# Kernel tuning notes

Measured on AMD Instinct MI355X. Metric: run time of the kernel, lower is better.

## Reference

```python
import jax, jax.numpy as jnp
import numpy as np

DIM = 128; HEADS = 8; WS = 8; SHIFT = 4; B = 8; H = 256; W = 256; T = 1


def _rel_index(ws):
    # faithful port of create_relative_position_index
    coords = np.arange(ws)
    yy, xx = np.meshgrid(coords, coords, indexing='ij')
    cf = np.stack([yy.reshape(-1), xx.reshape(-1)])          # (2, ws*ws)
    rel = cf[:, :, None] - cf[:, None, :]                     # (2, N, N)
    rel[0] += ws - 1
    rel[1] += ws - 1
    return rel[0] * (2 * ws - 1) + rel[1]                     # (N, N) int


def _row_mask(ws, shift):
    jj, ii = np.meshgrid(np.arange(ws), np.arange(ws), indexing='ij')
    return ((jj >= ws - shift) | (ii >= ws - shift)).reshape(-1)  # (N,) bool


def layernorm(x, g, b, eps=1e-5):
    mu = x.mean(-1, keepdims=True)
    var = ((x - mu) ** 2).mean(-1, keepdims=True)
    return (x - mu) * jax.lax.rsqrt(var + eps) * g + b


def setup_inputs() -> dict:
    key = jax.random.key(0)
    ks = jax.random.split(key, 16)
    s = 0.02
    d = DIM
    inp = {
        'x': jax.random.normal(ks[0], (B, T, H, W, d), jnp.float32),
        'wq': jax.random.normal(ks[1], (d, d), jnp.float32) * s,
        'bq': jnp.zeros((d,), jnp.float32),
        'wk': jax.random.normal(ks[2], (d, d), jnp.float32) * s,
        'bk': jnp.zeros((d,), jnp.float32),
        'wv': jax.random.normal(ks[3], (d, d), jnp.float32) * s,
        'bv': jnp.zeros((d,), jnp.float32),
        'wp': jax.random.normal(ks[4], (d, d), jnp.float32) * s,
        'bp': jnp.zeros((d,), jnp.float32),
        'rpb': jax.random.normal(ks[5], (2 * WS - 1, 2 * WS - 1, HEADS), jnp.float32) * s,
        'ln1_g': jnp.ones((d,), jnp.float32),
        'ln1_b': jnp.zeros((d,), jnp.float32),
        'ln2_g': jnp.ones((d,), jnp.float32),
        'ln2_b': jnp.zeros((d,), jnp.float32),
        'w1': jax.random.normal(ks[6], (d, 4 * d), jnp.float32) * s,
        'b1': jnp.zeros((4 * d,), jnp.float32),
        'w2': jax.random.normal(ks[7], (4 * d, d), jnp.float32) * s,
        'b2': jnp.zeros((d,), jnp.float32),
        'gate': jax.random.normal(ks[8], (1, H, W, 1), jnp.float32) * s,
    }
    return inp


def reference(x, wq, bq, wk, bk, wv, bv, wp, bp, rpb, ln1_g, ln1_b, ln2_g, ln2_b, w1, b1, w2, b2, gate):
    Bx, Tx, Hx, Wx, C = x.shape
    skip = x[:, 0]                                             # (B,H,W,C)
    xn = layernorm(x, ln1_g, ln1_b)[:, 0]                      # (B,H,W,C)
    xs = jnp.roll(xn, (-SHIFT, -SHIFT), axis=(1, 2))
    nh, nw, N = Hx // WS, Wx // WS, WS * WS
    # window partition -> (B*nh*nw, N, C)
    xw = xs.reshape(Bx, nh, WS, nw, WS, C).transpose(0, 1, 3, 2, 4, 5).reshape(-1, N, C)
    hd = C // HEADS
    scale = hd ** -0.5
    q = (xw @ wq + bq).reshape(-1, N, HEADS, hd)
    k = (xw @ wk + bk).reshape(-1, N, HEADS, hd)
    v = (xw @ wv + bv).reshape(-1, N, HEADS, hd)
    attn = jnp.einsum('bnhc,bmhc->bnhm', q, k) * scale         # (Bw,N,H,N)
    # relative position bias gather; .view(B,N,heads,N) over (N*N,heads) flat layout
    idx = jnp.asarray(_rel_index(WS).reshape(-1))
    bias = rpb.reshape(-1, HEADS)[idx].reshape(N, HEADS, N)
    attn = attn + bias[None]
    # shift mask: full query rows set to -1e9 (per original patch_mask)
    rmask = jnp.asarray(_row_mask(WS, SHIFT))
    attn = jnp.where(rmask[None, :, None, None], jnp.float32(-1e9), attn)
    attn = jax.nn.softmax(attn, axis=-1)
    out = jnp.einsum('bnhm,bmhc->bnhc', attn, v).reshape(-1, N, C) @ wp + bp
    # window reverse
    xr = out.reshape(Bx, nh, nw, WS, WS, C).transpose(0, 1, 3, 2, 4, 5).reshape(Bx, Hx, Wx, C)
    xa = xs + xr
    xa = jnp.roll(xa, (SHIFT, SHIFT), axis=(1, 2))
    # gated skip
    x2 = xa + jax.nn.sigmoid(gate) * skip
    # MLP (dropout = identity in eval)
    h = jax.nn.gelu(layernorm(x2, ln2_g, ln2_b) @ w1 + b1, approximate=False)
    y = x2 + (h @ w2 + b2)
    return y.reshape(Bx, Tx, Hx, Wx, C)
```

## Files before the change

kernel.cpp:

```cpp
#include <hip/hip_runtime.h>
#include <hip/hip_bf16.h>
#include <math.h>

#define TPB 256

typedef __attribute__((ext_vector_type(8))) __bf16 bf16x8;
typedef __attribute__((ext_vector_type(4))) __bf16 bf16x4;
typedef __attribute__((ext_vector_type(4))) float f32x4;

static __device__ __forceinline__ bf16x8 lds_frag(const char* base, int row, int byteOff, int rowBytes) {
    return *reinterpret_cast<const bf16x8*>(base + row * rowBytes + (byteOff ^ ((row & 7) << 4)));
}
static __device__ __forceinline__ void lds_wr4(char* base, int row, int col0, int rowBytes, f32x4 v) {
    bf16x4 p;
    p[0] = (__bf16)v[0]; p[1] = (__bf16)v[1]; p[2] = (__bf16)v[2]; p[3] = (__bf16)v[3];
    *reinterpret_cast<bf16x4*>(base + row * rowBytes + ((col0 << 1) ^ ((row & 7) << 4))) = p;
}

__global__ void convert_w(const float* __restrict__ wq, const float* __restrict__ wk,
                          const float* __restrict__ wv, const float* __restrict__ wp,
                          const float* __restrict__ w1, const float* __restrict__ w2,
                          const float* __restrict__ rpb, const float* __restrict__ bq,
                          __bf16* __restrict__ ws)
{
    int g = blockIdx.x * 256 + threadIdx.x;
    if (g < 65536) {
        int which = g >> 14, idx = g & 16383, n = idx >> 7, k = idx & 127;
        const float* W = (which == 0) ? wq : (which == 1) ? wk : (which == 2) ? wv : wp;
        float v = W[k * 128 + n];
        if (which == 0) v *= 0.25f;
        ws[g] = (__bf16)v;
    } else if (g < 131072) {
        int idx = g - 65536, n = idx >> 7, k = idx & 127;
        ws[g] = (__bf16)w1[k * 512 + n];
    } else if (g < 196608) {
        int idx = g - 131072, n = idx >> 9, k = idx & 511;
        ws[g] = (__bf16)w2[k * 128 + n];
    } else if (g < 204800) {
        float* wsf = (float*)(ws + 196608);
        int g2 = g - 196608;
        int hc = g2 >> 8, h = hc >> 2, ct = hc & 3;
        int lane = (g2 >> 2) & 63, kg = lane >> 4, ar = lane & 15, r = g2 & 3;
        int dy = (ar >> 2) - h + 7;
        int dx = (ar & 3) - (ct * 2 + (kg >> 1)) + 7;
        int hsrc = ((kg & 1) << 2) | r;
        wsf[g2] = rpb[(dy * 15 + dx) * 8 + hsrc];
    } else if (g < 204928) {
        float* wsf = (float*)(ws + 196608);
        wsf[8192 + (g - 204800)] = bq[g - 204800] * 0.25f;
    }
}

#define O_P     4096
#define O_ATTN  12288
#define O_MU    49152
#define O_RS    49408
#define O_GATE  49664
#define O_BASE  49920
#define O_VMEAN 50176
#define SMEM_SZ 50688

__global__ __launch_bounds__(TPB, 3) void swin_fused_kernel(
    const float* __restrict__ x,
    const __bf16* __restrict__ wqT,
    const __bf16* __restrict__ wkT, const float* __restrict__ bk,
    const __bf16* __restrict__ wvT, const float* __restrict__ bv,
    const __bf16* __restrict__ wpT, const float* __restrict__ bp,
    const float* __restrict__ bias_pre, const float* __restrict__ bqs,
    const float* __restrict__ ln1g, const float* __restrict__ ln1b,
    const float* __restrict__ ln2g, const float* __restrict__ ln2b,
    const __bf16* __restrict__ w1T, const float* __restrict__ b1,
    const __bf16* __restrict__ w2T, const float* __restrict__ b2,
    const float* __restrict__ gate,
    float* __restrict__ out)
{
    __shared__ __align__(16) char smem[SMEM_SZ];
    char* s_xn   = smem;
    char* s_q    = smem;
    char* s_k    = smem + 16384;
    char* s_vT   = smem + 32768;
    char* s_xn2  = smem + 32768;
    char* s_attn = smem + O_ATTN;
    char* s_h    = smem;
    float* s_proj = (float*)(smem);
    float* s_out  = (float*)(smem);
    float* s_mu   = (float*)(smem + O_MU);
    float* s_rs   = (float*)(smem + O_RS);
    float* s_gate = (float*)(smem + O_GATE);
    int*   s_base = (int*)(smem + O_BASE);
    float* s_vmean = (float*)(smem + O_VMEAN);

    const int tid = threadIdx.x;
    const int blk = blockIdx.x;
    const int b  = blk >> 10;
    const int wh = (blk >> 5) & 31;
    const int ww = blk & 31;

    const int row = tid >> 2;
    const int l4  = tid & 3;
    float vals[32];

    {
        const int si = wh * 8 + (row >> 3), sj = ww * 8 + (row & 7);
        const int oi = (si + 4) & 255, oj = (sj + 4) & 255;
        const int base = ((b * 256 + oi) * 256 + oj) * 128;
        if (l4 == 0) { s_base[row] = base; s_gate[row] = gate[oi * 256 + oj]; }
        const float* xp = x + base + l4 * 32;
        float sum = 0.f, sq = 0.f;
#pragma unroll
        for (int i = 0; i < 8; ++i) {
            const float4 v4 = reinterpret_cast<const float4*>(xp)[i];
            vals[4*i+0] = v4.x; vals[4*i+1] = v4.y; vals[4*i+2] = v4.z; vals[4*i+3] = v4.w;
            sum += v4.x + v4.y + v4.z + v4.w;
            sq  += v4.x*v4.x + v4.y*v4.y + v4.z*v4.z + v4.w*v4.w;
        }
        sum += __shfl_xor(sum, 1); sum += __shfl_xor(sum, 2);
        sq  += __shfl_xor(sq , 1); sq  += __shfl_xor(sq , 2);
        const float mu  = sum * (1.f / 128.f);
        const float var = sq * (1.f / 128.f) - mu * mu;
        const float rs  = rsqrtf(var + 1e-5f);
        if (l4 == 0) { s_mu[row] = mu; s_rs[row] = rs; }
#pragma unroll
        for (int j = 0; j < 4; ++j) {
            bf16x8 pk;
#pragma unroll
            for (int e = 0; e < 8; ++e) {
                const int d = l4 * 32 + j * 8 + e;
                pk[e] = (__bf16)((vals[j*8+e] - mu) * rs * ln1g[d] + ln1b[d]);
            }
            const int byteOff = (l4 * 64 + j * 16) ^ ((row & 7) << 4);
            *reinterpret_cast<bf16x8*>(s_xn + row * 256 + byteOff) = pk;
        }
    }
    __syncthreads();

    const int lane = tid & 63, w = tid >> 6;
    const int ar = lane & 15, kg = lane >> 4;

    bf16x8 a[4][4];
    bf16x8 aq[4];
    {
#pragma unroll
        for (int nt = 0; nt < 4; ++nt)
#pragma unroll
            for (int kc = 0; kc < 4; ++kc)
                a[nt][kc] = lds_frag(s_xn, nt * 16 + ar, kc * 64 + (kg << 4), 256);
        const int nrow = ((ar >> 2) << 3) + (ar & 3);
#pragma unroll
        for (int kc = 0; kc < 4; ++kc)
            aq[kc] = lds_frag(s_xn, nrow, kc * 64 + (kg << 4), 256);

#pragma unroll
        for (int ct2 = 0; ct2 < 2; ++ct2) {
            const int m0t = (w + ct2 * 4) * 16;
            bf16x8 af[4];
#pragma unroll
            for (int kc = 0; kc < 4; ++kc)
                af[kc] = *reinterpret_cast<const bf16x8*>(wkT + (m0t + ar) * 128 + kc * 32 + (kg << 3));
            const float4 bb4 = *reinterpret_cast<const float4*>(bk + m0t + kg * 4);
#pragma unroll
            for (int nt = 0; nt < 4; ++nt) {
                f32x4 c = {bb4.x, bb4.y, bb4.z, bb4.w};
#pragma unroll
                for (int kc = 0; kc < 4; ++kc)
                    c = __builtin_amdgcn_mfma_f32_16x16x32_bf16(af[kc], a[nt][kc], c, 0, 0, 0);
                lds_wr4(s_k, nt * 16 + ar, m0t + kg * 4, 256, c);
            }
        }
#pragma unroll
        for (int ct2 = 0; ct2 < 2; ++ct2) {
            const int brow = (w + ct2 * 4) * 16 + ar;
            bf16x8 bf[4];
#pragma unroll
            for (int kc = 0; kc < 4; ++kc)
                bf[kc] = *reinterpret_cast<const bf16x8*>(wvT + brow * 128 + kc * 32 + (kg << 3));
            const float bb = bv[brow];
            float vs = 0.f;
#pragma unroll
            for (int rt = 0; rt < 4; ++rt) {
                f32x4 c = {bb, bb, bb, bb};
#pragma unroll
                for (int kc = 0; kc < 4; ++kc)
                    c = __builtin_amdgcn_mfma_f32_16x16x32_bf16(a[rt][kc], bf[kc], c, 0, 0, 0);
                lds_wr4(s_vT, brow, rt * 16 + kg * 4, 128, c);
                vs += c[0] + c[1] + c[2] + c[3];
            }
            vs += __shfl_xor(vs, 16); vs += __shfl_xor(vs, 32);
            if (kg == 0) s_vmean[brow] = vs * (1.f / 64.f);
        }
    }
    __syncthreads();

    {
#pragma unroll
        for (int ct2 = 0; ct2 < 2; ++ct2) {
            const int m0t = (w + ct2 * 4) * 16;
            bf16x8 af[4];
#pragma unroll
            for (int kc = 0; kc < 4; ++kc)
                af[kc] = *reinterpret_cast<const bf16x8*>(wqT + (m0t + ar) * 128 + kc * 32 + (kg << 3));
            const float4 bb4 = *reinterpret_cast<const float4*>(bqs + m0t + kg * 4);
            f32x4 c = {bb4.x, bb4.y, bb4.z, bb4.w};
#pragma unroll
            for (int kc = 0; kc < 4; ++kc)
                c = __builtin_amdgcn_mfma_f32_16x16x32_bf16(af[kc], aq[kc], c, 0, 0, 0);
            lds_wr4(s_q, ar, m0t + kg * 4, 256, c);
        }
    }
    __syncthreads();

    char* s_p = smem + O_P + (w << 11);
#pragma unroll
    for (int hi = 0; hi < 2; ++hi) {
        const int h = w + hi * 4;
        bf16x8 aQ = {};
        if (lane < 32) aQ = lds_frag(s_q, ar, h * 32 + (kg << 4), 256);
        f32x4 sc[4];
#pragma unroll
        for (int ct = 0; ct < 4; ++ct) {
            bf16x8 bK = {};
            if (lane < 32) bK = lds_frag(s_k, ct * 16 + ar, h * 32 + (kg << 4), 256);
            const f32x4 cin = *reinterpret_cast<const f32x4*>(bias_pre + ((h * 4 + ct) << 8) + (lane << 2));
            sc[ct] = __builtin_amdgcn_mfma_f32_16x16x32_bf16(bK, aQ, cin, 0, 0, 0);
        }
        float sm = 0.f;
#pragma unroll
        for (int ct = 0; ct < 4; ++ct)
#pragma unroll
            for (int r = 0; r < 4; ++r) {
                sc[ct][r] = __expf(sc[ct][r]);
                sm += sc[ct][r];
            }
        sm += __shfl_xor(sm, 16); sm += __shfl_xor(sm, 32);
        const float inv = 1.f / sm;
#pragma unroll
        for (int ct = 0; ct < 4; ++ct) {
            f32x4 p4 = {sc[ct][0] * inv, sc[ct][1] * inv, sc[ct][2] * inv, sc[ct][3] * inv};
            lds_wr4(s_p, ar, ct * 16 + kg * 4, 128, p4);
        }
        f32x4 o = {0.f, 0.f, 0.f, 0.f};
#pragma unroll
        for (int kc = 0; kc < 2; ++kc) {
            bf16x8 ap = lds_frag(s_p,  ar, kc * 64 + (kg << 4), 128);
            bf16x8 bV = lds_frag(s_vT, h * 16 + ar, kc * 64 + (kg << 4), 128);
            o = __builtin_amdgcn_mfma_f32_16x16x32_bf16(bV, ap, o, 0, 0, 0);
        }
        lds_wr4(s_attn, ar, h * 16 + kg * 4, 256, o);
    }
    __syncthreads();

    {
        bf16x8 a2[4];
#pragma unroll
        for (int kc = 0; kc < 4; ++kc)
            a2[kc] = lds_frag(s_attn, ar, kc * 64 + (kg << 4), 256);
#pragma unroll
        for (int ct2 = 0; ct2 < 2; ++ct2) {
            const int brow = (w + ct2 * 4) * 16 + ar;
            bf16x8 bf[4];
#pragma unroll
            for (int kc = 0; kc < 4; ++kc)
                bf[kc] = *reinterpret_cast<const bf16x8*>(wpT + brow * 128 + kc * 32 + (kg << 3));
            const float bb = bp[brow];
            f32x4 c = {bb, bb, bb, bb};
#pragma unroll
            for (int kc = 0; kc < 4; ++kc)
                c = __builtin_amdgcn_mfma_f32_16x16x32_bf16(a2[kc], bf[kc], c, 0, 0, 0);
#pragma unroll
            for (int r = 0; r < 4; ++r)
                s_proj[(kg * 4 + r) * 132 + brow] = c[r];
        }
        if (tid < 128) {
            const int col = tid;
            float acc = bp[col];
#pragma unroll
            for (int j = 0; j < 16; ++j) {
                const bf16x8 w8 = *reinterpret_cast<const bf16x8*>(wpT + col * 128 + j * 8);
#pragma unroll
                for (int e = 0; e < 8; ++e)
                    acc += s_vmean[j * 8 + e] * (float)w8[e];
            }
            s_proj[16 * 132 + col] = acc;
        }
    }
    __syncthreads();

    {
        const float sg = 1.f / (1.f + __expf(-s_gate[row]));
        const float mu1 = s_mu[row], rs1 = s_rs[row];
        const bool masked = ((row >> 3) >= 4) || ((row & 7) >= 4);
        const int prow = masked ? 16 : ((row >> 3) * 4 + (row & 7));
        const float* pr = s_proj + prow * 132 + l4 * 32;
        const float* g1  = ln1g + l4 * 32;
        const float* b1v = ln1b + l4 * 32;
        float sum = 0.f, sq = 0.f;
#pragma unroll
        for (int i = 0; i < 8; ++i) {
            const float4 gg = reinterpret_cast<const float4*>(g1)[i];
            const float4 bb = reinterpret_cast<const float4*>(b1v)[i];
            const float g4[4] = {gg.x, gg.y, gg.z, gg.w};
            const float b4[4] = {bb.x, bb.y, bb.z, bb.w};
#pragma unroll
            for (int c = 0; c < 4; ++c) {
                const int idx = 4*i + c;
                const float xv = vals[idx];
                const float xnv = (xv - mu1) * rs1 * g4[c] + b4[c];
                const float x2 = xnv + pr[idx] + sg * xv;
                vals[idx] = x2;
                sum += x2; sq += x2 * x2;
            }
        }
        sum += __shfl_xor(sum, 1); sum += __shfl_xor(sum, 2);
        sq  += __shfl_xor(sq , 1); sq  += __shfl_xor(sq , 2);
        const float mu  = sum * (1.f / 128.f);
        const float var = sq * (1.f / 128.f) - mu * mu;
        const float rs  = rsqrtf(var + 1e-5f);
        __syncthreads();
#pragma unroll
        for (int j = 0; j < 4; ++j) {
            bf16x8 pk;
#pragma unroll
            for (int e = 0; e < 8; ++e) {
                const int d = l4 * 32 + j * 8 + e;
                pk[e] = (__bf16)((vals[j*8+e] - mu) * rs * ln2g[d] + ln2b[d]);
            }
            const int byteOff = (l4 * 64 + j * 16) ^ ((row & 7) << 4);
            *reinterpret_cast<bf16x8*>(s_xn2 + row * 256 + byteOff) = pk;
        }
    }
    __syncthreads();

    bf16x8 bx[4][4];
#pragma unroll
    for (int nt = 0; nt < 4; ++nt)
#pragma unroll
        for (int kc = 0; kc < 4; ++kc)
            bx[nt][kc] = lds_frag(s_xn2, nt * 16 + ar, kc * 64 + (kg << 4), 256);

    f32x4 acc2[2][4];
#pragma unroll
    for (int ct2 = 0; ct2 < 2; ++ct2) {
        const float bb = b2[(w + ct2 * 4) * 16 + ar];
#pragma unroll
        for (int rt = 0; rt < 4; ++rt) acc2[ct2][rt] = {bb, bb, bb, bb};
    }

#pragma unroll
    for (int hh = 0; hh < 2; ++hh) {
#pragma unroll
        for (int i = 0; i < 4; ++i) {
            const int hcol0 = (w + 4 * i) * 16;
            const int m0g = hh * 256 + hcol0;
            bf16x8 af[4];
#pragma unroll
            for (int kc = 0; kc < 4; ++kc)
                af[kc] = *reinterpret_cast<const bf16x8*>(w1T + (m0g + ar) * 128 + kc * 32 + (kg << 3));
            const float4 bb4 = *reinterpret_cast<const float4*>(b1 + m0g + kg * 4);
#pragma unroll
            for (int nt = 0; nt < 4; ++nt) {
                f32x4 c = {bb4.x, bb4.y, bb4.z, bb4.w};
#pragma unroll
                for (int kc = 0; kc < 4; ++kc)
                    c = __builtin_amdgcn_mfma_f32_16x16x32_bf16(af[kc], bx[nt][kc], c, 0, 0, 0);
                f32x4 g4;
#pragma unroll
                for (int r = 0; r < 4; ++r) {
                    const float v = c[r];
                    const float t = 0.7978845608028654f * (v + 0.044715f * v * v * v);
                    const float th = 1.f - 2.f / (__expf(2.f * t) + 1.f);
                    g4[r] = 0.5f * v * (1.f + th);
                }
                lds_wr4(s_h, nt * 16 + ar, hcol0 + kg * 4, 512, g4);
            }
        }
        __syncthreads();
#pragma unroll
        for (int kc = 0; kc < 8; ++kc) {
            bf16x8 ah[4];
#pragma unroll
            for (int rt = 0; rt < 4; ++rt)
                ah[rt] = lds_frag(s_h, rt * 16 + ar, kc * 64 + (kg << 4), 512);
#pragma unroll
            for (int ct2 = 0; ct2 < 2; ++ct2) {
                const int brow = (w + ct2 * 4) * 16 + ar;
                const bf16x8 bw = *reinterpret_cast<const bf16x8*>(w2T + brow * 512 + hh * 256 + kc * 32 + (kg << 3));
#pragma unroll
                for (int rt = 0; rt < 4; ++rt)
                    acc2[ct2][rt] = __builtin_amdgcn_mfma_f32_16x16x32_bf16(ah[rt], bw, acc2[ct2][rt], 0, 0, 0);
            }
        }
        __syncthreads();
    }

#pragma unroll
    for (int ct2 = 0; ct2 < 2; ++ct2)
#pragma unroll
        for (int rt = 0; rt < 4; ++rt)
#pragma unroll
            for (int r = 0; r < 4; ++r)
                s_out[(rt * 16 + kg * 4 + r) * 132 + (w + ct2 * 4) * 16 + ar] = acc2[ct2][rt][r];
    __syncthreads();
    {
        const int base = s_base[row];
        float* op = out + base + l4 * 32;
        const float* po = s_out + row * 132 + l4 * 32;
#pragma unroll
        for (int i = 0; i < 8; ++i) {
            float4 o;
            o.x = vals[4*i+0] + po[4*i+0];
            o.y = vals[4*i+1] + po[4*i+1];
            o.z = vals[4*i+2] + po[4*i+2];
            o.w = vals[4*i+3] + po[4*i+3];
            reinterpret_cast<float4*>(op)[i] = o;
        }
    }
}

extern "C" void kernel_launch(void* const* d_in, const int* in_sizes, int n_in,
                              void* d_out, int out_size, void* d_ws, size_t ws_size,
                              hipStream_t stream) {
    (void)in_sizes; (void)n_in; (void)ws_size; (void)out_size;
    const float* x    = (const float*)d_in[0];
    const float* wq   = (const float*)d_in[1];
    const float* bq   = (const float*)d_in[2];
    const float* wk   = (const float*)d_in[3];
    const float* bk   = (const float*)d_in[4];
    const float* wv   = (const float*)d_in[5];
    const float* bv   = (const float*)d_in[6];
    const float* wp   = (const float*)d_in[7];
    const float* bp   = (const float*)d_in[8];
    const float* rpb  = (const float*)d_in[9];
    const float* ln1g = (const float*)d_in[10];
    const float* ln1b = (const float*)d_in[11];
    const float* ln2g = (const float*)d_in[12];
    const float* ln2b = (const float*)d_in[13];
    const float* w1   = (const float*)d_in[14];
    const float* b1   = (const float*)d_in[15];
    const float* w2   = (const float*)d_in[16];
    const float* b2   = (const float*)d_in[17];
    const float* gate = (const float*)d_in[18];
    float* out = (float*)d_out;

    __bf16* ws = (__bf16*)d_ws;
    const __bf16* wqT = ws;
    const __bf16* wkT = ws + 16384;
    const __bf16* wvT = ws + 32768;
    const __bf16* wpT = ws + 49152;
    const __bf16* w1T = ws + 65536;
    const __bf16* w2T = ws + 131072;
    const float* wsf  = (const float*)(ws + 196608);
    const float* bias_pre = wsf;
    const float* bqs      = wsf + 8192;

    convert_w<<<801, 256, 0, stream>>>(wq, wk, wv, wp, w1, w2, rpb, bq, ws);
    swin_fused_kernel<<<8192, TPB, 0, stream>>>(x, wqT, wkT, bk, wvT, bv, wpT, bp,
                                                bias_pre, bqs, ln1g, ln1b, ln2g, ln2b,
                                                w1T, b1, w2T, b2, gate, out);
}
```

Before: 745.8 us.

## Double block size to 512 threads, one head per wave, simplified GELU

Doubles the threads per block from 256 to 512 so each of the 8 waves owns one head and one 16-column tile in the QKV, projection and MLP GEMMs. Each thread now handles 16 channels instead of 32. The K and V projections are fused into one loop that reloads activation fragments from LDS per tile instead of keeping a 4x4 fragment array in registers. The smem layout is enlarged so the P buffers no longer alias, and one barrier is removed from the LN2 phase. GELU uses a sigmoid form with a fast reciprocal, and the softmax uses rcp. This is meant to cut register pressure and raise parallelism per window, at the cost of larger LDS use, a lower occupancy bound of 2, and more LDS fragment reads.

Result: slower. 776.7 us (+4.1%).

```diff
diff --git a/kernel.cpp b/kernel.cpp
--- a/kernel.cpp
+++ b/kernel.cpp
@@ -2,7 +2,7 @@
 #include <hip/hip_bf16.h>
 #include <math.h>
 
-#define TPB 256
+#define TPB 512
 
 typedef __attribute__((ext_vector_type(8))) __bf16 bf16x8;
 typedef __attribute__((ext_vector_type(4))) __bf16 bf16x4;
@@ -51,16 +51,18 @@
     }
 }
 
-#define O_P     4096
 #define O_ATTN  12288
-#define O_MU    49152
-#define O_RS    49408
-#define O_GATE  49664
-#define O_BASE  49920
-#define O_VMEAN 50176
-#define SMEM_SZ 50688
-
-__global__ __launch_bounds__(TPB, 3) void swin_fused_kernel(
+#define O_K     16384
+#define O_VT    32768
+#define O_P     49152
+#define O_MU    65536
+#define O_RS    65792
+#define O_GATE  66048
+#define O_BASE  66304
+#define O_VMEAN 66560
+#define SMEM_SZ 67072
+
+__global__ __launch_bounds__(TPB, 2) void swin_fused_kernel(
     const float* __restrict__ x,
     const __bf16* __restrict__ wqT,
     const __bf16* __restrict__ wkT, const float* __restrict__ bk,
@@ -77,10 +79,10 @@
     __shared__ __align__(16) char smem[SMEM_SZ];
     char* s_xn   = smem;
     char* s_q    = smem;
-    char* s_k    = smem + 16384;
-    char* s_vT   = smem + 32768;
-    char* s_xn2  = smem + 32768;
     char* s_attn = smem + O_ATTN;
+    char* s_k    = smem + O_K;
+    char* s_vT   = smem + O_VT;
+    char* s_xn2  = smem + O_VT;
     char* s_h    = smem;
     float* s_proj = (float*)(smem);
     float* s_out  = (float*)(smem);
@@ -96,39 +98,39 @@
     const int wh = (blk >> 5) & 31;
     const int ww = blk & 31;
 
-    const int row = tid >> 2;
-    const int l4  = tid & 3;
-    float vals[32];
+    const int row = tid >> 3;
+    const int l8  = tid & 7;
+    float vals[16];
 
     {
         const int si = wh * 8 + (row >> 3), sj = ww * 8 + (row & 7);
         const int oi = (si + 4) & 255, oj = (sj + 4) & 255;
         const int base = ((b * 256 + oi) * 256 + oj) * 128;
-        if (l4 == 0) { s_base[row] = base; s_gate[row] = gate[oi * 256 + oj]; }
-        const float* xp = x + base + l4 * 32;
+        if (l8 == 0) { s_base[row] = base; s_gate[row] = gate[oi * 256 + oj]; }
+        const float* xp = x + base + l8 * 16;
         float sum = 0.f, sq = 0.f;
 #pragma unroll
-        for (int i = 0; i < 8; ++i) {
+        for (int i = 0; i < 4; ++i) {
             const float4 v4 = reinterpret_cast<const float4*>(xp)[i];
             vals[4*i+0] = v4.x; vals[4*i+1] = v4.y; vals[4*i+2] = v4.z; vals[4*i+3] = v4.w;
             sum += v4.x + v4.y + v4.z + v4.w;
             sq  += v4.x*v4.x + v4.y*v4.y + v4.z*v4.z + v4.w*v4.w;
         }
-        sum += __shfl_xor(sum, 1); sum += __shfl_xor(sum, 2);
-        sq  += __shfl_xor(sq , 1); sq  += __shfl_xor(sq , 2);
+        sum += __shfl_xor(sum, 1); sum += __shfl_xor(sum, 2); sum += __shfl_xor(sum, 4);
+        sq  += __shfl_xor(sq , 1); sq  += __shfl_xor(sq , 2); sq  += __shfl_xor(sq , 4);
         const float mu  = sum * (1.f / 128.f);
         const float var = sq * (1.f / 128.f) - mu * mu;
         const float rs  = rsqrtf(var + 1e-5f);
-        if (l4 == 0) { s_mu[row] = mu; s_rs[row] = rs; }
-#pragma unroll
-        for (int j = 0; j < 4; ++j) {
+        if (l8 == 0) { s_mu[row] = mu; s_rs[row] = rs; }
+#pragma unroll
+        for (int j = 0; j < 2; ++j) {
             bf16x8 pk;
 #pragma unroll
             for (int e = 0; e < 8; ++e) {
-                const int d = l4 * 32 + j * 8 + e;
+                const int d = l8 * 16 + j * 8 + e;
                 pk[e] = (__bf16)((vals[j*8+e] - mu) * rs * ln1g[d] + ln1b[d]);
             }
-            const int byteOff = (l4 * 64 + j * 16) ^ ((row & 7) << 4);
+            const int byteOff = (l8 * 32 + j * 16) ^ ((row & 7) << 4);
             *reinterpret_cast<bf16x8*>(s_xn + row * 256 + byteOff) = pk;
         }
     }
@@ -137,82 +139,66 @@
     const int lane = tid & 63, w = tid >> 6;
     const int ar = lane & 15, kg = lane >> 4;
 
-    bf16x8 a[4][4];
     bf16x8 aq[4];
-    {
-#pragma unroll
-        for (int nt = 0; nt < 4; ++nt)
+
+    {
+        const int nrow = ((ar >> 2) << 3) + (ar & 3);
+#pragma unroll
+        for (int kc = 0; kc < 4; ++kc)
+            aq[kc] = lds_frag(s_xn, nrow, kc * 64 + (kg << 4), 256);
+
+        const int m0t = w * 16;
+        const int brow = w * 16 + ar;
+        bf16x8 afk[4], bfv[4];
+#pragma unroll
+        for (int kc = 0; kc < 4; ++kc) {
+            afk[kc] = *reinterpret_cast<const bf16x8*>(wkT + (m0t + ar) * 128 + kc * 32 + (kg << 3));
+            bfv[kc] = *reinterpret_cast<const bf16x8*>(wvT + brow * 128 + kc * 32 + (kg << 3));
+        }
+        const float4 bbk = *reinterpret_cast<const float4*>(bk + m0t + kg * 4);
+        const float bbv = bv[brow];
+        float vs = 0.f;
+#pragma unroll
+        for (int nt = 0; nt < 4; ++nt) {
+            bf16x8 bx[4];
 #pragma unroll
             for (int kc = 0; kc < 4; ++kc)
-                a[nt][kc] = lds_frag(s_xn, nt * 16 + ar, kc * 64 + (kg << 4), 256);
-        const int nrow = ((ar >> 2) << 3) + (ar & 3);
-#pragma unroll
-        for (int kc = 0; kc < 4; ++kc)
-            aq[kc] = lds_frag(s_xn, nrow, kc * 64 + (kg << 4), 256);
-
-#pragma unroll
-        for (int ct2 = 0; ct2 < 2; ++ct2) {
-            const int m0t = (w + ct2 * 4) * 16;
-            bf16x8 af[4];
+                bx[kc] = lds_frag(s_xn, nt * 16 + ar, kc * 64 + (kg << 4), 256);
+            f32x4 ck = {bbk.x, bbk.y, bbk.z, bbk.w};
 #pragma unroll
             for (int kc = 0; kc < 4; ++kc)
-                af[kc] = *reinterpret_cast<const bf16x8*>(wkT + (m0t + ar) * 128 + kc * 32 + (kg << 3));
-            const float4 bb4 = *reinterpret_cast<const float4*>(bk + m0t + kg * 4);
-#pragma unroll
-            for (int nt = 0; nt < 4; ++nt) {
-                f32x4 c = {bb4.x, bb4.y, bb4.z, bb4.w};
-#pragma unroll
-                for (int kc = 0; kc < 4; ++kc)
-                    c = __builtin_amdgcn_mfma_f32_16x16x32_bf16(af[kc], a[nt][kc], c, 0, 0, 0);
-                lds_wr4(s_k, nt * 16 + ar, m0t + kg * 4, 256, c);
-            }
-        }
-#pragma unroll
-        for (int ct2 = 0; ct2 < 2; ++ct2) {
-            const int brow = (w + ct2 * 4) * 16 + ar;
-            bf16x8 bf[4];
+                ck = __builtin_amdgcn_mfma_f32_16x16x32_bf16(afk[kc], bx[kc], ck, 0, 0, 0);
+            lds_wr4(s_k, nt * 16 + ar, m0t + kg * 4, 256, ck);
+            f32x4 cv = {bbv, bbv, bbv, bbv};
 #pragma unroll
             for (int kc = 0; kc < 4; ++kc)
-                bf[kc] = *reinterpret_cast<const bf16x8*>(wvT + brow * 128 + kc * 32 + (kg << 3));
-            const float bb = bv[brow];
-            float vs = 0.f;
-#pragma unroll
-            for (int rt = 0; rt < 4; ++rt) {
-                f32x4 c = {bb, bb, bb, bb};
-#pragma unroll
-                for (int kc = 0; kc < 4; ++kc)
-                    c = __builtin_amdgcn_mfma_f32_16x16x32_bf16(a[rt][kc], bf[kc], c, 0, 0, 0);
-                lds_wr4(s_vT, brow, rt * 16 + kg * 4, 128, c);
-                vs += c[0] + c[1] + c[2] + c[3];
-            }
-            vs += __shfl_xor(vs, 16); vs += __shfl_xor(vs, 32);
-            if (kg == 0) s_vmean[brow] = vs * (1.f / 64.f);
-        }
-    }
-    __syncthreads();
-
-    {
-#pragma unroll
-        for (int ct2 = 0; ct2 < 2; ++ct2) {
-            const int m0t = (w + ct2 * 4) * 16;
-            bf16x8 af[4];
-#pragma unroll
-            for (int kc = 0; kc < 4; ++kc)
-                af[kc] = *reinterpret_cast<const bf16x8*>(wqT + (m0t + ar) * 128 + kc * 32 + (kg << 3));
-            const float4 bb4 = *reinterpret_cast<const float4*>(bqs + m0t + kg * 4);
-            f32x4 c = {bb4.x, bb4.y, bb4.z, bb4.w};
-#pragma unroll
-            for (int kc = 0; kc < 4; ++kc)
-                c = __builtin_amdgcn_mfma_f32_16x16x32_bf16(af[kc], aq[kc], c, 0, 0, 0);
-            lds_wr4(s_q, ar, m0t + kg * 4, 256, c);
-        }
-    }
-    __syncthreads();
-
-    char* s_p = smem + O_P + (w << 11);
-#pragma unroll
-    for (int hi = 0; hi < 2; ++hi) {
-        const int h = w + hi * 4;
+                cv = __builtin_amdgcn_mfma_f32_16x16x32_bf16(bx[kc], bfv[kc], cv, 0, 0, 0);
+            lds_wr4(s_vT, brow, nt * 16 + kg * 4, 128, cv);
+            vs += cv[0] + cv[1] + cv[2] + cv[3];
+        }
+        vs += __shfl_xor(vs, 16); vs += __shfl_xor(vs, 32);
+        if (kg == 0) s_vmean[brow] = vs * (1.f / 64.f);
+    }
+    __syncthreads();
+
+    {
+        const int m0t = w * 16;
+        bf16x8 af[4];
+#pragma unroll
+        for (int kc = 0; kc < 4; ++kc)
+            af[kc] = *reinterpret_cast<const bf16x8*>(wqT + (m0t + ar) * 128 + kc * 32 + (kg << 3));
+        const float4 bb4 = *reinterpret_cast<const float4*>(bqs + m0t + kg * 4);
+        f32x4 c = {bb4.x, bb4.y, bb4.z, bb4.w};
+#pragma unroll
+        for (int kc = 0; kc < 4; ++kc)
+            c = __builtin_amdgcn_mfma_f32_16x16x32_bf16(af[kc], aq[kc], c, 0, 0, 0);
+        lds_wr4(s_q, ar, m0t + kg * 4, 256, c);
+    }
+    __syncthreads();
+
+    {
+        const int h = w;
+        char* s_p = smem + O_P + (w << 11);
         bf16x8 aQ = {};
         if (lane < 32) aQ = lds_frag(s_q, ar, h * 32 + (kg << 4), 256);
         f32x4 sc[4];
@@ -232,7 +218,7 @@
                 sm += sc[ct][r];
             }
         sm += __shfl_xor(sm, 16); sm += __shfl_xor(sm, 32);
-        const float inv = 1.f / sm;
+        const float inv = __builtin_amdgcn_rcpf(sm);
 #pragma unroll
         for (int ct = 0; ct < 4; ++ct) {
             f32x4 p4 = {sc[ct][0] * inv, sc[ct][1] * inv, sc[ct][2] * inv, sc[ct][3] * inv};
@@ -254,22 +240,19 @@
 #pragma unroll
         for (int kc = 0; kc < 4; ++kc)
             a2[kc] = lds_frag(s_attn, ar, kc * 64 + (kg << 4), 256);
-#pragma unroll
-        for (int ct2 = 0; ct2 < 2; ++ct2) {
-            const int brow = (w + ct2 * 4) * 16 + ar;
-            bf16x8 bf[4];
-#pragma unroll
-            for (int kc = 0; kc < 4; ++kc)
-                bf[kc] = *reinterpret_cast<const bf16x8*>(wpT + brow * 128 + kc * 32 + (kg << 3));
-            const float bb = bp[brow];
-            f32x4 c = {bb, bb, bb, bb};
-#pragma unroll
-            for (int kc = 0; kc < 4; ++kc)
-                c = __builtin_amdgcn_mfma_f32_16x16x32_bf16(a2[kc], bf[kc], c, 0, 0, 0);
-#pragma unroll
-            for (int r = 0; r < 4; ++r)
-                s_proj[(kg * 4 + r) * 132 + brow] = c[r];
-        }
+        const int brow = w * 16 + ar;
+        bf16x8 bf[4];
+#pragma unroll
+        for (int kc = 0; kc < 4; ++kc)
+            bf[kc] = *reinterpret_cast<const bf16x8*>(wpT + brow * 128 + kc * 32 + (kg << 3));
+        const float bb = bp[brow];
+        f32x4 c = {bb, bb, bb, bb};
+#pragma unroll
+        for (int kc = 0; kc < 4; ++kc)
+            c = __builtin_amdgcn_mfma_f32_16x16x32_bf16(a2[kc], bf[kc], c, 0, 0, 0);
+#pragma unroll
+        for (int r = 0; r < 4; ++r)
+            s_proj[(kg * 4 + r) * 132 + brow] = c[r];
         if (tid < 128) {
             const int col = tid;
             float acc = bp[col];
@@ -290,12 +273,12 @@
         const float mu1 = s_mu[row], rs1 = s_rs[row];
         const bool masked = ((row >> 3) >= 4) || ((row & 7) >= 4);
         const int prow = masked ? 16 : ((row >> 3) * 4 + (row & 7));
-        const float* pr = s_proj + prow * 132 + l4 * 32;
-        const float* g1  = ln1g + l4 * 32;
-        const float* b1v = ln1b + l4 * 32;
+        const float* pr = s_proj + prow * 132 + l8 * 16;
+        const float* g1  = ln1g + l8 * 16;
+        const float* b1v = ln1b + l8 * 16;
         float sum = 0.f, sq = 0.f;
 #pragma unroll
-        for (int i = 0; i < 8; ++i) {
+        for (int i = 0; i < 4; ++i) {
             const float4 gg = reinterpret_cast<const float4*>(g1)[i];
             const float4 bb = reinterpret_cast<const float4*>(b1v)[i];
             const float g4[4] = {gg.x, gg.y, gg.z, gg.w};
@@ -310,67 +293,70 @@
                 sum += x2; sq += x2 * x2;
             }
         }
-        sum += __shfl_xor(sum, 1); sum += __shfl_xor(sum, 2);
-        sq  += __shfl_xor(sq , 1); sq  += __shfl_xor(sq , 2);
+        sum += __shfl_xor(sum, 1); sum += __shfl_xor(sum, 2); sum += __shfl_xor(sum, 4);
+        sq  += __shfl_xor(sq , 1); sq  += __shfl_xor(sq , 2); sq  += __shfl_xor(sq , 4);
         const float mu  = sum * (1.f / 128.f);
         const float var = sq * (1.f / 128.f) - mu * mu;
         const float rs  = rsqrtf(var + 1e-5f);
-        __syncthreads();
-#pragma unroll
-        for (int j = 0; j < 4; ++j) {
+#pragma unroll
+        for (int j = 0; j < 2; ++j) {
             bf16x8 pk;
 #pragma unroll
             for (int e = 0; e < 8; ++e) {
-                const int d = l4 * 32 + j * 8 + e;
+                const int d = l8 * 16 + j * 8 + e;
                 pk[e] = (__bf16)((vals[j*8+e] - mu) * rs * ln2g[d] + ln2b[d]);
             }
-            const int byteOff = (l4 * 64 + j * 16) ^ ((row & 7) << 4);
+            const int byteOff = (l8 * 32 + j * 16) ^ ((row & 7) << 4);
             *reinterpret_cast<bf16x8*>(s_xn2 + row * 256 + byteOff) = pk;
         }
     }
     __syncthreads();
 
-    bf16x8 bx[4][4];
-#pragma unroll
-    for (int nt = 0; nt < 4; ++nt)
-#pragma unroll
-        for (int kc = 0; kc < 4; ++kc)
-            bx[nt][kc] = lds_frag(s_xn2, nt * 16 + ar, kc * 64 + (kg << 4), 256);
-
-    f32x4 acc2[2][4];
-#pragma unroll
-    for (int ct2 = 0; ct2 < 2; ++ct2) {
-        const float bb = b2[(w + ct2 * 4) * 16 + ar];
-#pragma unroll
-        for (int rt = 0; rt < 4; ++rt) acc2[ct2][rt] = {bb, bb, bb, bb};
+    const int brow2 = w * 16 + ar;
+    f32x4 acc2[4];
+    {
+        const float bb = b2[brow2];
+#pragma unroll
+        for (int rt = 0; rt < 4; ++rt) acc2[rt] = {bb, bb, bb, bb};
     }
 
 #pragma unroll
     for (int hh = 0; hh < 2; ++hh) {
-#pragma unroll
-        for (int i = 0; i < 4; ++i) {
-            const int hcol0 = (w + 4 * i) * 16;
-            const int m0g = hh * 256 + hcol0;
-            bf16x8 af[4];
+        bf16x8 af0[4], af1[4];
+        float4 bbh0, bbh1;
+        {
+            const int m0a = hh * 256 + w * 16;
+            const int m0b = hh * 256 + (w + 8) * 16;
+#pragma unroll
+            for (int kc = 0; kc < 4; ++kc) {
+                af0[kc] = *reinterpret_cast<const bf16x8*>(w1T + (m0a + ar) * 128 + kc * 32 + (kg << 3));
+                af1[kc] = *reinterpret_cast<const bf16x8*>(w1T + (m0b + ar) * 128 + kc * 32 + (kg << 3));
+            }
+            bbh0 = *reinterpret_cast<const float4*>(b1 + m0a + kg * 4);
+            bbh1 = *reinterpret_cast<const float4*>(b1 + m0b + kg * 4);
+        }
+#pragma unroll
+        for (int nt = 0; nt < 4; ++nt) {
+            bf16x8 bx[4];
 #pragma unroll
             for (int kc = 0; kc < 4; ++kc)
-                af[kc] = *reinterpret_cast<const bf16x8*>(w1T + (m0g + ar) * 128 + kc * 32 + (kg << 3));
-            const float4 bb4 = *reinterpret_cast<const float4*>(b1 + m0g + kg * 4);
-#pragma unroll
-            for (int nt = 0; nt < 4; ++nt) {
+                bx[kc] = lds_frag(s_xn2, nt * 16 + ar, kc * 64 + (kg << 4), 256);
+#pragma unroll
+            for (int ti = 0; ti < 2; ++ti) {
+                const float4 bb4 = ti ? bbh1 : bbh0;
                 f32x4 c = {bb4.x, bb4.y, bb4.z, bb4.w};
 #pragma unroll
                 for (int kc = 0; kc < 4; ++kc)
-                    c = __builtin_amdgcn_mfma_f32_16x16x32_bf16(af[kc], bx[nt][kc], c, 0, 0, 0);
+                    c = __builtin_amdgcn_mfma_f32_16x16x32_bf16(ti ? af1[kc] : af0[kc], bx[kc], c, 0, 0, 0);
                 f32x4 g4;
 #pragma unroll
                 for (int r = 0; r < 4; ++r) {
                     const float v = c[r];
-                    const float t = 0.7978845608028654f * (v + 0.044715f * v * v * v);
-                    const float th = 1.f - 2.f / (__expf(2.f * t) + 1.f);
-                    g4[r] = 0.5f * v * (1.f + th);
+                    const float u = v * fmaf(0.044715f, v * v, 1.0f);
+                    const float e = __expf(-1.5957691216057308f * u);
+                    g4[r] = v * __builtin_amdgcn_rcpf(1.0f + e);
                 }
-                lds_wr4(s_h, nt * 16 + ar, hcol0 + kg * 4, 512, g4);
+                lds_wr4(s_h, nt * 16 + ar, (w + ti * 8) * 16 + kg * 4, 512, g4);
             }
         }
         __syncthreads();
@@ -380,32 +366,26 @@
 #pragma unroll
             for (int rt = 0; rt < 4; ++rt)
                 ah[rt] = lds_frag(s_h, rt * 16 + ar, kc * 64 + (kg << 4), 512);
-#pragma unroll
-            for (int ct2 = 0; ct2 < 2; ++ct2) {
-                const int brow = (w + ct2 * 4) * 16 + ar;
-                const bf16x8 bw = *reinterpret_cast<const bf16x8*>(w2T + brow * 512 + hh * 256 + kc * 32 + (kg << 3));
-#pragma unroll
-                for (int rt = 0; rt < 4; ++rt)
-                    acc2[ct2][rt] = __builtin_amdgcn_mfma_f32_16x16x32_bf16(ah[rt], bw, acc2[ct2][rt], 0, 0, 0);
-            }
+            const bf16x8 bw = *reinterpret_cast<const bf16x8*>(w2T + brow2 * 512 + hh * 256 + kc * 32 + (kg << 3));
+#pragma unroll
+            for (int rt = 0; rt < 4; ++rt)
+                acc2[rt] = __builtin_amdgcn_mfma_f32_16x16x32_bf16(ah[rt], bw, acc2[rt], 0, 0, 0);
         }
         __syncthreads();
     }
 
 #pragma unroll
-    for (int ct2 = 0; ct2 < 2; ++ct2)
-#pragma unroll
-        for (int rt = 0; rt < 4; ++rt)
-#pragma unroll
-            for (int r = 0; r < 4; ++r)
-                s_out[(rt * 16 + kg * 4 + r) * 132 + (w + ct2 * 4) * 16 + ar] = acc2[ct2][rt][r];
+    for (int rt = 0; rt < 4; ++rt)
+#pragma unroll
+        for (int r = 0; r < 4; ++r)
+            s_out[(rt * 16 + kg * 4 + r) * 132 + brow2] = acc2[rt][r];
     __syncthreads();
     {
         const int base = s_base[row];
-        float* op = out + base + l4 * 32;
-        const float* po = s_out + row * 132 + l4 * 32;
-#pragma unroll
-        for (int i = 0; i < 8; ++i) {
+        float* op = out + base + l8 * 16;
+        const float* po = s_out + row * 132 + l8 * 16;
+#pragma unroll
+        for (int i = 0; i < 4; ++i) {
             float4 o;
             o.x = vals[4*i+0] + po[4*i+0];
             o.y = vals[4*i+1] + po[4*i+1];
```
